# Performance work log

Hardware: AMD Instinct MI355X
Metric: run time of the kernel (lower is better)

## Reference

```python
import jax, jax.numpy as jnp
import numpy as np

N_ATOMS = 200000
N_BONDS = 400000
MAX_NB = 6
HID = 128
ATOM_FDIM = 151
BOND_FDIM = 165
N_HEADS = 2


def _layer_norm(x, g, b, eps=1e-5):
    mu = jnp.mean(x, axis=-1, keepdims=True)
    var = jnp.var(x, axis=-1, keepdims=True)
    return g * (x - mu) * jax.lax.rsqrt(var + eps) + b


def setup_inputs() -> dict:
    key = jax.random.key(0)
    ks = jax.random.split(key, 12)
    s = 0.05  # weight init scale
    return {
        'f_atoms': jax.random.normal(ks[0], (N_ATOMS, ATOM_FDIM), jnp.float32),
        'f_bonds': jax.random.normal(ks[1], (N_BONDS, BOND_FDIM), jnp.float32),
        'a2a': jax.random.randint(ks[2], (N_ATOMS, MAX_NB), 0, N_ATOMS, jnp.int32),
        'a2b': jax.random.randint(ks[3], (N_ATOMS, MAX_NB), 0, N_BONDS, jnp.int32),
        'W_i': jax.random.normal(ks[4], (ATOM_FDIM, HID), jnp.float32) * s,
        'b_i': jnp.zeros((HID,), jnp.float32),
        'ln1_g': jnp.ones((HID,), jnp.float32),
        'ln1_b': jnp.zeros((HID,), jnp.float32),
        'Wh_q': jax.random.normal(ks[5], (N_HEADS, HID + BOND_FDIM, HID), jnp.float32) * s,
        'bh_q': jnp.zeros((N_HEADS, HID), jnp.float32),
        'Wh_k': jax.random.normal(ks[6], (N_HEADS, HID + BOND_FDIM, HID), jnp.float32) * s,
        'bh_k': jnp.zeros((N_HEADS, HID), jnp.float32),
        'Wh_v': jax.random.normal(ks[7], (N_HEADS, HID + BOND_FDIM, HID), jnp.float32) * s,
        'bh_v': jnp.zeros((N_HEADS, HID), jnp.float32),
        'W_o': jax.random.normal(ks[8], (N_HEADS * HID, HID), jnp.float32) * s,
        'b_o': jnp.zeros((HID,), jnp.float32),
        'ln2_g': jnp.ones((HID,), jnp.float32),
        'ln2_b': jnp.zeros((HID,), jnp.float32),
    }


def reference(f_atoms, f_bonds, a2a, a2b, W_i, b_i, ln1_g, ln1_b,
              Wh_q, bh_q, Wh_k, bh_k, Wh_v, bh_v, W_o, b_o, ln2_g, ln2_b):
    # Input projection of raw atom features: dropout(layernorm(act(W_i x)))
    # (dropout = identity in eval).
    h0 = _layer_norm(jax.nn.relu(f_atoms @ W_i + b_i), ln1_g, ln1_b)  # [N, H]

    # Graph gather: neighbor atom hidden states + incident bond raw features.
    nei_a = h0[a2a]       # [N, nb, H]   irregular gather
    nei_b = f_bonds[a2b]  # [N, nb, Fb]  irregular gather
    # Aggregate messages once; shared across Q/K/V branches and heads.
    msg = jnp.concatenate([nei_a, nei_b], axis=-1).sum(axis=1)  # [N, H+Fb]

    def branch(Wh, bh):  # Wh: [heads, H+Fb, H] -> [N, heads, H]
        return jax.nn.relu(h0[:, None, :] + jnp.einsum('nf,efh->neh', msg, Wh) + bh)

    Q = branch(Wh_q, bh_q)  # [N, heads, H]
    K = branch(Wh_k, bh_k)
    V = branch(Wh_v, bh_v)

    # Attention across the heads axis (per atom).
    scores = jnp.einsum('nqh,nkh->nqk', Q, K) / jnp.sqrt(jnp.float32(HID))
    attn = jax.nn.softmax(scores, axis=-1)
    x = jnp.einsum('nqk,nkh->nqh', attn, V).reshape(Q.shape[0], -1)  # [N, heads*H]

    x_out = x @ W_o + b_o  # [N, H]
    # Residual sublayer connection.
    f_atoms_out = h0 + _layer_norm(x_out, ln2_g, ln2_b)
    return f_atoms_out
```

## Files before the change

kernel.cpp:

```cpp
#include <hip/hip_runtime.h>

typedef unsigned short u16;
typedef unsigned int u32;
typedef __attribute__((ext_vector_type(8))) short s8v;
typedef __attribute__((ext_vector_type(4))) float f4v;
typedef __attribute__((ext_vector_type(2))) float f2v;

#define NATOMS 200000
#define NBONDS 400000

__device__ __forceinline__ float b2f(u32 u) {
    union { u32 i; float f; } v; v.i = u << 16; return v.f;
}
__device__ __forceinline__ u16 f2b(float f) {
    union { float f; u32 i; } v; v.f = f;
    u32 r = v.i + 0x7fffu + ((v.i >> 16) & 1u);
    return (u16)(r >> 16);
}
__device__ __forceinline__ uint4 pack8(const float* f) {
    uint4 o;
    o.x = (u32)f2b(f[0]) | ((u32)f2b(f[1]) << 16);
    o.y = (u32)f2b(f[2]) | ((u32)f2b(f[3]) << 16);
    o.z = (u32)f2b(f[4]) | ((u32)f2b(f[5]) << 16);
    o.w = (u32)f2b(f[6]) | ((u32)f2b(f[7]) << 16);
    return o;
}
__device__ __forceinline__ void acc8(uint4 u, float* a) {
    a[0] += b2f(u.x & 0xffffu); a[1] += b2f(u.x >> 16);
    a[2] += b2f(u.y & 0xffffu); a[3] += b2f(u.y >> 16);
    a[4] += b2f(u.z & 0xffffu); a[5] += b2f(u.z >> 16);
    a[6] += b2f(u.w & 0xffffu); a[7] += b2f(u.w >> 16);
}

template<int C>
__device__ __forceinline__ float dpp_mov_f(float x) {
    return __int_as_float(__builtin_amdgcn_update_dpp(
        0, __float_as_int(x), C, 0xF, 0xF, true));
}
__device__ __forceinline__ float red8(float x) {
    x += dpp_mov_f<0xB1>(x);
    x += dpp_mov_f<0x4E>(x);
    x += dpp_mov_f<0x141>(x);
    return x;
}
__device__ __forceinline__ float red16(float x) {
    x += dpp_mov_f<0xB1>(x);
    x += dpp_mov_f<0x4E>(x);
    x += dpp_mov_f<0x141>(x);
    x += dpp_mov_f<0x128>(x);
    return x;
}

__global__ void k_wprep(const float* __restrict__ Whq, const float* __restrict__ Whk,
                        const float* __restrict__ Whv, const float* __restrict__ Wo,
                        const float* __restrict__ Wi,
                        u16* __restrict__ wallw, u16* __restrict__ wow, u16* __restrict__ wiw) {
    int t = blockIdx.x * 256 + threadIdx.x;
    if (t < 245760) {
        int ks = t / 24576, rem = t % 24576;
        int n = rem >> 5, kk = rem & 31;
        int k = ks * 32 + kk;
        int hg = n / 48, r48 = n % 48;
        int branch = r48 >> 4, r16i = r48 & 15;
        int head = r16i >> 3, h = hg * 8 + (r16i & 7);
        const float* Wp = (branch == 0) ? Whq : ((branch == 1) ? Whk : Whv);
        float val = (k < 293) ? Wp[(head * 293 + k) * 128 + h] : 0.f;
        wallw[t] = f2b(val);
    } else if (t < 278528) {
        int u = t - 245760;
        int ks = u >> 12, n = (u >> 5) & 127, kk = u & 31;
        int k = ks * 32 + kk;
        wow[u] = f2b(Wo[k * 128 + n]);
    } else if (t < 299008) {
        int u = t - 278528;
        int ks = u >> 12, n = (u >> 5) & 127, kk = u & 31;
        int k = ks * 32 + kk;
        wiw[u] = (k < 151) ? f2b(Wi[k * 128 + n]) : (u16)0;
    }
}

__global__ void k_bond16(const float* __restrict__ fb, u16* __restrict__ fbw) {
    int t = blockIdx.x * 256 + threadIdx.x;
    if (t >= NBONDS * 21) return;
    u32 b = (u32)t / 21u, c = (u32)t % 21u;
    const float* src = fb + (size_t)b * 165 + c * 8;
    float a[8];
    #pragma unroll
    for (int q = 0; q < 8; q++) a[q] = ((int)(c * 8 + q) < 165) ? src[q] : 0.f;
    *(uint4*)&fbw[(size_t)b * 168 + c * 8] = pack8(a);
}

__global__ void k_msgab(const u16* __restrict__ h0w, const int* __restrict__ a2a,
                        u16* __restrict__ msga,
                        const u16* __restrict__ fbw, const int* __restrict__ a2b,
                        u16* __restrict__ msgb) {
    if (blockIdx.x < 12500) {
        int t = blockIdx.x * 256 + threadIdx.x;
        if (t >= NATOMS * 16) return;
        u32 atom = (u32)t >> 4, c = (u32)t & 15u;
        const int* na = a2a + (size_t)atom * 6;
        float a[8] = {0, 0, 0, 0, 0, 0, 0, 0};
        #pragma unroll
        for (int j = 0; j < 6; j++)
            acc8(*(const uint4*)&h0w[(size_t)(u32)na[j] * 128 + c * 8], a);
        *(uint4*)&msga[(size_t)atom * 128 + c * 8] = pack8(a);
    } else {
        int t = (blockIdx.x - 12500) * 256 + threadIdx.x;
        if (t >= NATOMS * 21) return;
        u32 atom = (u32)t / 21u, c = (u32)t % 21u;
        const int* nb = a2b + (size_t)atom * 6;
        float a[8] = {0, 0, 0, 0, 0, 0, 0, 0};
        #pragma unroll
        for (int j = 0; j < 6; j++)
            acc8(*(const uint4*)&fbw[(size_t)(u32)nb[j] * 168 + c * 8], a);
        *(uint4*)&msgb[(size_t)atom * 168 + c * 8] = pack8(a);
    }
}

#define H0_SMEM (64 * 168 * 2 + 64 * 132 * 4)
__global__ __launch_bounds__(256) void k_h0(
    const float* __restrict__ fa, const u16* __restrict__ wiw,
    const float* __restrict__ bi, const float* __restrict__ g1, const float* __restrict__ b1,
    u16* __restrict__ h0w) {
    extern __shared__ char smem[];
    u16* la = (u16*)smem;
    float* lo = (float*)(smem + 21504);
    const int tid = threadIdx.x;
    const size_t abase = (size_t)blockIdx.x * 64;

    for (int i = tid; i < 64 * 151; i += 256) {
        int r = i / 151, c = i - r * 151;
        la[r * 168 + c] = f2b(fa[(abase + r) * 151 + c]);
    }
    for (int i = tid; i < 64 * 17; i += 256) {
        int r = i / 17, c = i - r * 17;
        la[r * 168 + 151 + c] = 0;
    }
    __syncthreads();

    const int w = tid >> 6, l = tid & 63;
    const int r16 = l & 15, kq = l >> 4;
    f4v acc[4][2];
    #pragma unroll
    for (int m = 0; m < 4; m++)
        #pragma unroll
        for (int c = 0; c < 2; c++)
            #pragma unroll
            for (int v = 0; v < 4; v++) acc[m][c][v] = 0.f;

    #pragma unroll
    for (int ks = 0; ks < 5; ++ks) {
        s8v af[4];
        #pragma unroll
        for (int m = 0; m < 4; m++)
            af[m] = *(const s8v*)&la[(m * 16 + r16) * 168 + ks * 32 + kq * 8];
        #pragma unroll
        for (int c = 0; c < 2; c++) {
            int n = w * 32 + c * 16 + r16;
            s8v bf = *(const s8v*)&wiw[ks * 4096 + n * 32 + kq * 8];
            #pragma unroll
            for (int m = 0; m < 4; m++)
                acc[m][c] = __builtin_amdgcn_mfma_f32_16x16x32_bf16(af[m], bf, acc[m][c], 0, 0, 0);
        }
    }
    #pragma unroll
    for (int c = 0; c < 2; c++) {
        int col = w * 32 + c * 16 + r16;
        float bias = bi[col];
        #pragma unroll
        for (int m = 0; m < 4; m++) {
            #pragma unroll
            for (int v = 0; v < 4; v++) {
                int row = m * 16 + kq * 4 + v;
                lo[row * 132 + col] = fmaxf(acc[m][c][v] + bias, 0.f);
            }
        }
    }
    __syncthreads();

    const int ga = tid >> 2, sb = tid & 3;
    float vals[32], s = 0.f, s2 = 0.f;
    #pragma unroll
    for (int j = 0; j < 32; j++) {
        float v = lo[ga * 132 + sb + 4 * j];
        vals[j] = v; s += v; s2 += v * v;
    }
    s += dpp_mov_f<0xB1>(s); s += dpp_mov_f<0x4E>(s);
    s2 += dpp_mov_f<0xB1>(s2); s2 += dpp_mov_f<0x4E>(s2);
    float mu = s * (1.f / 128.f), var = s2 * (1.f / 128.f) - mu * mu;
    float rs = rsqrtf(var + 1e-5f);
    u16* orow = h0w + (abase + ga) * 128;
    #pragma unroll
    for (int j = 0; j < 32; j++) {
        int col = sb + 4 * j;
        orow[col] = f2b(g1[col] * (vals[j] - mu) * rs + b1[col]);
    }
}

#define SMEM_FUSED 39936
__global__ __launch_bounds__(1024, 8) void k_fused(
    const u16* __restrict__ h0w, const u16* __restrict__ msga, const u16* __restrict__ msgb,
    const u16* __restrict__ wallw, const u16* __restrict__ wow,
    const float* __restrict__ bhq, const float* __restrict__ bhk, const float* __restrict__ bhv,
    const float* __restrict__ bo, const float* __restrict__ g2, const float* __restrict__ b2,
    float* __restrict__ out) {
    extern __shared__ char smem[];
    u16* lx = (u16*)smem;
    float* sco2 = (float*)(smem + 20480);
    u16* lh0 = (u16*)(smem + 28672);
    float* attn = (float*)(smem + 37376);
    float* pp = (float*)(smem + 37888);

    const int tid = threadIdx.x;
    const size_t abase = (size_t)blockIdx.x * 32;
    const int w = tid >> 6, l = tid & 63;
    const int r16 = l & 15, kq = l >> 4;
    const u32 xmask = (u32)((r16 & 7) << 4);

    const u16* bp = wallw + (size_t)(w * 48 + r16) * 32 + kq * 8;
    s8v bfA0 = *(const s8v*)&bp[0];
    s8v bfA1 = *(const s8v*)&bp[512];
    s8v bfA2 = *(const s8v*)&bp[1024];

    if (tid < 512) {
        int r = tid >> 4, c8 = tid & 15;
        *(uint4*)&lh0[r * 136 + c8 * 8] = *(const uint4*)&h0w[(abase + r) * 128 + c8 * 8];
    }

    #pragma unroll
    for (int ii = 0; ii < 2; ++ii) {
        int i = tid + ii * 1024;
        if (i < 1280) {
            int r = i / 40, c = i - r * 40;
            uint4 val;
            if (c < 16) {
                val = *(const uint4*)&msga[(abase + r) * 128 + c * 8];
            } else if (c < 37) {
                val = *(const uint4*)&msgb[(abase + r) * 168 + (c - 16) * 8];
            } else {
                val = (uint4){0, 0, 0, 0};
            }
            *(uint4*)(smem + (((u32)(r * 640 + c * 16)) ^ ((u32)((r & 7) << 4)))) = val;
        }
    }
    __syncthreads();

    f4v acc[2][3];
    #pragma unroll
    for (int m = 0; m < 2; m++)
        #pragma unroll
        for (int c = 0; c < 3; c++)
            #pragma unroll
            for (int v = 0; v < 4; v++) acc[m][c][v] = 0.f;

    s8v bfB0, bfB1, bfB2;
    #pragma unroll
    for (int kp = 0; kp < 5; ++kp) {
        {
            const int ks = 2 * kp;
            const u16* nb = bp + (size_t)(ks + 1) * 24576;
            bfB0 = *(const s8v*)&nb[0];
            bfB1 = *(const s8v*)&nb[512];
            bfB2 = *(const s8v*)&nb[1024];
            #pragma unroll
            for (int m = 0; m < 2; m++) {
                s8v af = *(const s8v*)(smem +
                    (((u32)((m * 16 + r16) * 640 + ks * 64 + kq * 16)) ^ xmask));
                acc[m][0] = __builtin_amdgcn_mfma_f32_16x16x32_bf16(af, bfA0, acc[m][0], 0, 0, 0);
                acc[m][1] = __builtin_amdgcn_mfma_f32_16x16x32_bf16(af, bfA1, acc[m][1], 0, 0, 0);
                acc[m][2] = __builtin_amdgcn_mfma_f32_16x16x32_bf16(af, bfA2, acc[m][2], 0, 0, 0);
            }
        }
        {
            const int ks = 2 * kp + 1;
            if (kp < 4) {
                const u16* nb = bp + (size_t)(ks + 1) * 24576;
                bfA0 = *(const s8v*)&nb[0];
                bfA1 = *(const s8v*)&nb[512];
                bfA2 = *(const s8v*)&nb[1024];
            }
            #pragma unroll
            for (int m = 0; m < 2; m++) {
                s8v af = *(const s8v*)(smem +
                    (((u32)((m * 16 + r16) * 640 + ks * 64 + kq * 16)) ^ xmask));
                acc[m][0] = __builtin_amdgcn_mfma_f32_16x16x32_bf16(af, bfB0, acc[m][0], 0, 0, 0);
                acc[m][1] = __builtin_amdgcn_mfma_f32_16x16x32_bf16(af, bfB1, acc[m][1], 0, 0, 0);
                acc[m][2] = __builtin_amdgcn_mfma_f32_16x16x32_bf16(af, bfB2, acc[m][2], 0, 0, 0);
            }
        }
    }

    const int head = r16 >> 3;
    const int h = w * 8 + (r16 & 7);
    const float bq = bhq[head * 128 + h];
    const float bk = bhk[head * 128 + h];
    const float bv = bhv[head * 128 + h];
    #pragma unroll
    for (int m = 0; m < 2; m++) {
        #pragma unroll
        for (int v = 0; v < 4; v++) {
            int row = m * 16 + kq * 4 + v;
            float h0v = b2f(lh0[row * 136 + h]);
            float q  = fmaxf(acc[m][0][v] + h0v + bq, 0.f);
            float kk = fmaxf(acc[m][1][v] + h0v + bk, 0.f);
            float vv = fmaxf(acc[m][2][v] + h0v + bv, 0.f);
            acc[m][2][v] = vv;
            float kx = dpp_mov_f<0x128>(kk);
            float pA = red8(q * kk);
            float pB = red8(q * kx);
            if ((r16 & 7) == (m * 4 + v)) {
                f2v pr; pr[0] = pA; pr[1] = pB;
                *(f2v*)&sco2[(w * 32 + row) * 4 + head * 2] = pr;
            }
        }
    }
    __syncthreads();

    if (tid < 64) {
        int atom = tid >> 1, qh = tid & 1;
        float ss = 0.f, sx = 0.f;
        #pragma unroll
        for (int ww = 0; ww < 16; ww++) {
            f2v p = *(const f2v*)&sco2[(ww * 32 + atom) * 4 + qh * 2];
            ss += p[0]; sx += p[1];
        }
        const float sc = 0.08838834764831845f;
        ss *= sc; sx *= sc;
        float mm = fmaxf(ss, sx);
        float e0 = __expf(ss - mm), e1 = __expf(sx - mm);
        float inv = 1.f / (e0 + e1);
        attn[atom * 4 + qh * 2] = e0 * inv;
        attn[atom * 4 + qh * 2 + 1] = e1 * inv;
    }
    __syncthreads();

    #pragma unroll
    for (int m = 0; m < 2; m++) {
        #pragma unroll
        for (int v = 0; v < 4; v++) {
            int row = m * 16 + kq * 4 + v;
            f2v a = *(const f2v*)&attn[row * 4 + head * 2];
            float vv = acc[m][2][v];
            float vx = dpp_mov_f<0x128>(vv);
            lx[row * 264 + head * 128 + h] = f2b(a[0] * vv + a[1] * vx);
        }
    }
    __syncthreads();

    const int mb = w >> 3, ch = w & 7;
    f4v oa;
    #pragma unroll
    for (int v = 0; v < 4; v++) oa[v] = 0.f;
    const u16* xp = lx + (mb * 16 + r16) * 264 + kq * 8;
    const u16* wp2 = wow + (ch * 16 + r16) * 32 + kq * 8;
    #pragma unroll
    for (int ks = 0; ks < 8; ks++) {
        s8v a = *(const s8v*)&xp[ks * 32];
        s8v b = *(const s8v*)&wp2[ks * 4096];
        oa = __builtin_amdgcn_mfma_f32_16x16x32_bf16(a, b, oa, 0, 0, 0);
    }

    const int col = ch * 16 + r16;
    const float boc = bo[col];
    float xo[4];
    #pragma unroll
    for (int v = 0; v < 4; v++) {
        xo[v] = oa[v] + boc;
        float s = red16(xo[v]);
        float s2 = red16(xo[v] * xo[v]);
        if (r16 == 0) {
            int row = mb * 16 + kq * 4 + v;
            f2v pr; pr[0] = s; pr[1] = s2;
            *(f2v*)&pp[(row * 8 + ch) * 2] = pr;
        }
    }
    __syncthreads();

    const float gac = g2[col], bbc = b2[col];
    #pragma unroll
    for (int v = 0; v < 4; v++) {
        int row = mb * 16 + kq * 4 + v;
        f4v p0 = *(f4v*)&pp[row * 16];
        f4v p1 = *(f4v*)&pp[row * 16 + 4];
        f4v p2 = *(f4v*)&pp[row * 16 + 8];
        f4v p3 = *(f4v*)&pp[row * 16 + 12];
        float ssum = p0[0] + p0[2] + p1[0] + p1[2] + p2[0] + p2[2] + p3[0] + p3[2];
        float s2sum = p0[1] + p0[3] + p1[1] + p1[3] + p2[1] + p2[3] + p3[1] + p3[3];
        float mu = ssum * (1.f / 128.f);
        float var = s2sum * (1.f / 128.f) - mu * mu;
        float rs = rsqrtf(var + 1e-5f);
        out[(abase + row) * 128 + col] =
            gac * (xo[v] - mu) * rs + bbc + b2f(lh0[row * 136 + col]);
    }
}

extern "C" void kernel_launch(void* const* d_in, const int* in_sizes, int n_in,
                              void* d_out, int out_size, void* d_ws, size_t ws_size,
                              hipStream_t stream) {
    const float* f_atoms = (const float*)d_in[0];
    const float* f_bonds = (const float*)d_in[1];
    const int* a2a = (const int*)d_in[2];
    const int* a2b = (const int*)d_in[3];
    const float* W_i = (const float*)d_in[4];
    const float* b_i = (const float*)d_in[5];
    const float* ln1g = (const float*)d_in[6];
    const float* ln1b = (const float*)d_in[7];
    const float* Whq = (const float*)d_in[8];
    const float* bhq = (const float*)d_in[9];
    const float* Whk = (const float*)d_in[10];
    const float* bhk = (const float*)d_in[11];
    const float* Whv = (const float*)d_in[12];
    const float* bhv = (const float*)d_in[13];
    const float* Wo = (const float*)d_in[14];
    const float* bo = (const float*)d_in[15];
    const float* ln2g = (const float*)d_in[16];
    const float* ln2b = (const float*)d_in[17];
    float* out = (float*)d_out;

    char* ws = (char*)d_ws;
    u16* h0w = (u16*)(ws + 0);
    u16* fbw = (u16*)(ws + 51200000);
    u16* msga = (u16*)(ws + 185600000);
    u16* msgb = (u16*)(ws + 236800000);
    u16* wallw = (u16*)(ws + 304000000);
    u16* wow = (u16*)(ws + 304491520);
    u16* wiw = (u16*)(ws + 304557056);

    hipFuncSetAttribute(reinterpret_cast<const void*>(k_fused),
                        hipFuncAttributeMaxDynamicSharedMemorySize, SMEM_FUSED);

    k_wprep<<<1168, 256, 0, stream>>>(Whq, Whk, Whv, Wo, W_i, wallw, wow, wiw);
    k_bond16<<<32813, 256, 0, stream>>>(f_bonds, fbw);
    k_h0<<<3125, 256, H0_SMEM, stream>>>(f_atoms, wiw, b_i, ln1g, ln1b, h0w);
    k_msgab<<<28907, 256, 0, stream>>>(h0w, a2a, msga, fbw, a2b, msgb);
    k_fused<<<6250, 1024, SMEM_FUSED, stream>>>(h0w, msga, msgb, wallw, wow,
                                                bhq, bhk, bhv, bo, ln2g, ln2b, out);
}
```

Baseline: 572.3 us.

## Process 48 atoms per block in fused kernel to amortize weight loads

```diff
diff --git a/kernel.cpp b/kernel.cpp
--- a/kernel.cpp
+++ b/kernel.cpp
@@ -37,16 +37,19 @@
     return __int_as_float(__builtin_amdgcn_update_dpp(
         0, __float_as_int(x), C, 0xF, 0xF, true));
 }
+__device__ __forceinline__ float swz_xor4(float x) {
+    return __int_as_float(__builtin_amdgcn_ds_swizzle(__float_as_int(x), 0x101F));
+}
 __device__ __forceinline__ float red8(float x) {
     x += dpp_mov_f<0xB1>(x);
     x += dpp_mov_f<0x4E>(x);
-    x += dpp_mov_f<0x141>(x);
+    x += swz_xor4(x);
     return x;
 }
 __device__ __forceinline__ float red16(float x) {
     x += dpp_mov_f<0xB1>(x);
     x += dpp_mov_f<0x4E>(x);
-    x += dpp_mov_f<0x141>(x);
+    x += swz_xor4(x);
     x += dpp_mov_f<0x128>(x);
     return x;
 }
@@ -197,7 +200,7 @@
     }
 }
 
-#define SMEM_FUSED 39936
+#define SMEM_FUSED 34560
 __global__ __launch_bounds__(1024, 8) void k_fused(
     const u16* __restrict__ h0w, const u16* __restrict__ msga, const u16* __restrict__ msgb,
     const u16* __restrict__ wallw, const u16* __restrict__ wow,
@@ -205,38 +208,28 @@
     const float* __restrict__ bo, const float* __restrict__ g2, const float* __restrict__ b2,
     float* __restrict__ out) {
     extern __shared__ char smem[];
+    float* sco2 = (float*)smem;
     u16* lx = (u16*)smem;
-    float* sco2 = (float*)(smem + 20480);
-    u16* lh0 = (u16*)(smem + 28672);
-    float* attn = (float*)(smem + 37376);
-    float* pp = (float*)(smem + 37888);
+    float* attn = (float*)(smem + 30720);
+    float* pp = (float*)(smem + 31488);
 
     const int tid = threadIdx.x;
-    const size_t abase = (size_t)blockIdx.x * 32;
+    const int abase = blockIdx.x * 48;
     const int w = tid >> 6, l = tid & 63;
     const int r16 = l & 15, kq = l >> 4;
     const u32 xmask = (u32)((r16 & 7) << 4);
 
-    const u16* bp = wallw + (size_t)(w * 48 + r16) * 32 + kq * 8;
-    s8v bfA0 = *(const s8v*)&bp[0];
-    s8v bfA1 = *(const s8v*)&bp[512];
-    s8v bfA2 = *(const s8v*)&bp[1024];
-
-    if (tid < 512) {
-        int r = tid >> 4, c8 = tid & 15;
-        *(uint4*)&lh0[r * 136 + c8 * 8] = *(const uint4*)&h0w[(abase + r) * 128 + c8 * 8];
-    }
-
     #pragma unroll
     for (int ii = 0; ii < 2; ++ii) {
         int i = tid + ii * 1024;
-        if (i < 1280) {
+        if (i < 1920) {
             int r = i / 40, c = i - r * 40;
+            int rr = abase + r; if (rr >= NATOMS) rr = NATOMS - 1;
             uint4 val;
             if (c < 16) {
-                val = *(const uint4*)&msga[(abase + r) * 128 + c * 8];
+                val = *(const uint4*)&msga[(size_t)rr * 128 + c * 8];
             } else if (c < 37) {
-                val = *(const uint4*)&msgb[(abase + r) * 168 + (c - 16) * 8];
+                val = *(const uint4*)&msgb[(size_t)rr * 168 + (c - 16) * 8];
             } else {
                 val = (uint4){0, 0, 0, 0};
             }
@@ -245,50 +238,31 @@
     }
     __syncthreads();
 
-    f4v acc[2][3];
-    #pragma unroll
-    for (int m = 0; m < 2; m++)
+    f4v acc[3][3];
+    #pragma unroll
+    for (int m = 0; m < 3; m++)
         #pragma unroll
         for (int c = 0; c < 3; c++)
             #pragma unroll
             for (int v = 0; v < 4; v++) acc[m][c][v] = 0.f;
 
-    s8v bfB0, bfB1, bfB2;
-    #pragma unroll
-    for (int kp = 0; kp < 5; ++kp) {
-        {
-            const int ks = 2 * kp;
-            const u16* nb = bp + (size_t)(ks + 1) * 24576;
-            bfB0 = *(const s8v*)&nb[0];
-            bfB1 = *(const s8v*)&nb[512];
-            bfB2 = *(const s8v*)&nb[1024];
-            #pragma unroll
-            for (int m = 0; m < 2; m++) {
-                s8v af = *(const s8v*)(smem +
-                    (((u32)((m * 16 + r16) * 640 + ks * 64 + kq * 16)) ^ xmask));
-                acc[m][0] = __builtin_amdgcn_mfma_f32_16x16x32_bf16(af, bfA0, acc[m][0], 0, 0, 0);
-                acc[m][1] = __builtin_amdgcn_mfma_f32_16x16x32_bf16(af, bfA1, acc[m][1], 0, 0, 0);
-                acc[m][2] = __builtin_amdgcn_mfma_f32_16x16x32_bf16(af, bfA2, acc[m][2], 0, 0, 0);
-            }
-        }
-        {
-            const int ks = 2 * kp + 1;
-            if (kp < 4) {
-                const u16* nb = bp + (size_t)(ks + 1) * 24576;
-                bfA0 = *(const s8v*)&nb[0];
-                bfA1 = *(const s8v*)&nb[512];
-                bfA2 = *(const s8v*)&nb[1024];
-            }
-            #pragma unroll
-            for (int m = 0; m < 2; m++) {
-                s8v af = *(const s8v*)(smem +
-                    (((u32)((m * 16 + r16) * 640 + ks * 64 + kq * 16)) ^ xmask));
-                acc[m][0] = __builtin_amdgcn_mfma_f32_16x16x32_bf16(af, bfB0, acc[m][0], 0, 0, 0);
-                acc[m][1] = __builtin_amdgcn_mfma_f32_16x16x32_bf16(af, bfB1, acc[m][1], 0, 0, 0);
-                acc[m][2] = __builtin_amdgcn_mfma_f32_16x16x32_bf16(af, bfB2, acc[m][2], 0, 0, 0);
-            }
-        }
-    }
+    const u16* bp = wallw + (size_t)(w * 48 + r16) * 32 + kq * 8;
+    #pragma unroll
+    for (int ks = 0; ks < 10; ++ks) {
+        const u16* nb = bp + (size_t)ks * 24576;
+        s8v b0 = *(const s8v*)&nb[0];
+        s8v b1 = *(const s8v*)&nb[512];
+        s8v b2_ = *(const s8v*)&nb[1024];
+        #pragma unroll
+        for (int m = 0; m < 3; m++) {
+            s8v af = *(const s8v*)(smem +
+                (((u32)((m * 16 + r16) * 640 + ks * 64 + kq * 16)) ^ xmask));
+            acc[m][0] = __builtin_amdgcn_mfma_f32_16x16x32_bf16(af, b0, acc[m][0], 0, 0, 0);
+            acc[m][1] = __builtin_amdgcn_mfma_f32_16x16x32_bf16(af, b1, acc[m][1], 0, 0, 0);
+            acc[m][2] = __builtin_amdgcn_mfma_f32_16x16x32_bf16(af, b2_, acc[m][2], 0, 0, 0);
+        }
+    }
+    __syncthreads();
 
     const int head = r16 >> 3;
     const int h = w * 8 + (r16 & 7);
@@ -296,11 +270,12 @@
     const float bk = bhk[head * 128 + h];
     const float bv = bhv[head * 128 + h];
     #pragma unroll
-    for (int m = 0; m < 2; m++) {
+    for (int m = 0; m < 3; m++) {
         #pragma unroll
         for (int v = 0; v < 4; v++) {
             int row = m * 16 + kq * 4 + v;
-            float h0v = b2f(lh0[row * 136 + h]);
+            int gr = abase + row; if (gr >= NATOMS) gr = NATOMS - 1;
+            float h0v = b2f(h0w[(size_t)gr * 128 + h]);
             float q  = fmaxf(acc[m][0][v] + h0v + bq, 0.f);
             float kk = fmaxf(acc[m][1][v] + h0v + bk, 0.f);
             float vv = fmaxf(acc[m][2][v] + h0v + bv, 0.f);
@@ -308,20 +283,20 @@
             float kx = dpp_mov_f<0x128>(kk);
             float pA = red8(q * kk);
             float pB = red8(q * kx);
-            if ((r16 & 7) == (m * 4 + v)) {
+            if ((r16 & 7) == ((m * 4 + v) & 7)) {
                 f2v pr; pr[0] = pA; pr[1] = pB;
-                *(f2v*)&sco2[(w * 32 + row) * 4 + head * 2] = pr;
-            }
-        }
-    }
-    __syncthreads();
-
-    if (tid < 64) {
+                *(f2v*)&sco2[(w * 48 + row) * 4 + head * 2] = pr;
+            }
+        }
+    }
+    __syncthreads();
+
+    if (tid < 96) {
         int atom = tid >> 1, qh = tid & 1;
         float ss = 0.f, sx = 0.f;
         #pragma unroll
         for (int ww = 0; ww < 16; ww++) {
-            f2v p = *(const f2v*)&sco2[(ww * 32 + atom) * 4 + qh * 2];
+            f2v p = *(const f2v*)&sco2[(ww * 48 + atom) * 4 + qh * 2];
             ss += p[0]; sx += p[1];
         }
         const float sc = 0.08838834764831845f;
@@ -335,7 +310,7 @@
     __syncthreads();
 
     #pragma unroll
-    for (int m = 0; m < 2; m++) {
+    for (int m = 0; m < 3; m++) {
         #pragma unroll
         for (int v = 0; v < 4; v++) {
             int row = m * 16 + kq * 4 + v;
@@ -347,50 +322,69 @@
     }
     __syncthreads();
 
-    const int mb = w >> 3, ch = w & 7;
-    f4v oa;
-    #pragma unroll
-    for (int v = 0; v < 4; v++) oa[v] = 0.f;
-    const u16* xp = lx + (mb * 16 + r16) * 264 + kq * 8;
+    const int ch = w & 7;
+    const int nmb = (w < 8) ? 2 : 1;
+    const int mb0 = (w < 8) ? 0 : 2;
+    f4v oa[2];
+    #pragma unroll
+    for (int v = 0; v < 4; v++) { oa[0][v] = 0.f; oa[1][v] = 0.f; }
     const u16* wp2 = wow + (ch * 16 + r16) * 32 + kq * 8;
     #pragma unroll
     for (int ks = 0; ks < 8; ks++) {
-        s8v a = *(const s8v*)&xp[ks * 32];
         s8v b = *(const s8v*)&wp2[ks * 4096];
-        oa = __builtin_amdgcn_mfma_f32_16x16x32_bf16(a, b, oa, 0, 0, 0);
+        #pragma unroll
+        for (int i = 0; i < 2; i++) {
+            if (i < nmb) {
+                s8v a = *(const s8v*)&lx[((mb0 + i) * 16 + r16) * 264 + ks * 32 + kq * 8];
+                oa[i] = __builtin_amdgcn_mfma_f32_16x16x32_bf16(a, b, oa[i], 0, 0, 0);
+            }
+        }
     }
 
     const int col = ch * 16 + r16;
     const float boc = bo[col];
-    float xo[4];
-    #pragma unroll
-    for (int v = 0; v < 4; v++) {
-        xo[v] = oa[v] + boc;
-        float s = red16(xo[v]);
-        float s2 = red16(xo[v] * xo[v]);
-        if (r16 == 0) {
-            int row = mb * 16 + kq * 4 + v;
-            f2v pr; pr[0] = s; pr[1] = s2;
-            *(f2v*)&pp[(row * 8 + ch) * 2] = pr;
+    float xo[2][4];
+    #pragma unroll
+    for (int i = 0; i < 2; i++) {
+        if (i < nmb) {
+            #pragma unroll
+            for (int v = 0; v < 4; v++) {
+                xo[i][v] = oa[i][v] + boc;
+                float s = red16(xo[i][v]);
+                float s2 = red16(xo[i][v] * xo[i][v]);
+                if (r16 == 0) {
+                    int row = (mb0 + i) * 16 + kq * 4 + v;
+                    f2v pr; pr[0] = s; pr[1] = s2;
+                    *(f2v*)&pp[(row * 8 + ch) * 2] = pr;
+                }
+            }
         }
     }
     __syncthreads();
 
     const float gac = g2[col], bbc = b2[col];
     #pragma unroll
-    for (int v = 0; v < 4; v++) {
-        int row = mb * 16 + kq * 4 + v;
-        f4v p0 = *(f4v*)&pp[row * 16];
-        f4v p1 = *(f4v*)&pp[row * 16 + 4];
-        f4v p2 = *(f4v*)&pp[row * 16 + 8];
-        f4v p3 = *(f4v*)&pp[row * 16 + 12];
-        float ssum = p0[0] + p0[2] + p1[0] + p1[2] + p2[0] + p2[2] + p3[0] + p3[2];
-        float s2sum = p0[1] + p0[3] + p1[1] + p1[3] + p2[1] + p2[3] + p3[1] + p3[3];
-        float mu = ssum * (1.f / 128.f);
-        float var = s2sum * (1.f / 128.f) - mu * mu;
-        float rs = rsqrtf(var + 1e-5f);
-        out[(abase + row) * 128 + col] =
-            gac * (xo[v] - mu) * rs + bbc + b2f(lh0[row * 136 + col]);
+    for (int i = 0; i < 2; i++) {
+        if (i < nmb) {
+            #pragma unroll
+            for (int v = 0; v < 4; v++) {
+                int row = (mb0 + i) * 16 + kq * 4 + v;
+                f4v p0 = *(f4v*)&pp[row * 16];
+                f4v p1 = *(f4v*)&pp[row * 16 + 4];
+                f4v p2 = *(f4v*)&pp[row * 16 + 8];
+                f4v p3 = *(f4v*)&pp[row * 16 + 12];
+                float ssum = p0[0] + p0[2] + p1[0] + p1[2] + p2[0] + p2[2] + p3[0] + p3[2];
+                float s2sum = p0[1] + p0[3] + p1[1] + p1[3] + p2[1] + p2[3] + p3[1] + p3[3];
+                float mu = ssum * (1.f / 128.f);
+                float var = s2sum * (1.f / 128.f) - mu * mu;
+                float rs = rsqrtf(var + 1e-5f);
+                int gr = abase + row;
+                if (gr < NATOMS) {
+                    out[(size_t)gr * 128 + col] =
+                        gac * (xo[i][v] - mu) * rs + bbc + b2f(h0w[(size_t)gr * 128 + col]);
+                }
+            }
+        }
     }
 }
 
@@ -433,6 +427,6 @@
     k_bond16<<<32813, 256, 0, stream>>>(f_bonds, fbw);
     k_h0<<<3125, 256, H0_SMEM, stream>>>(f_atoms, wiw, b_i, ln1g, ln1b, h0w);
     k_msgab<<<28907, 256, 0, stream>>>(h0w, a2a, msga, fbw, a2b, msgb);
-    k_fused<<<6250, 1024, SMEM_FUSED, stream>>>(h0w, msga, msgb, wallw, wow,
+    k_fused<<<4167, 1024, SMEM_FUSED, stream>>>(h0w, msga, msgb, wallw, wow,
                                                 bhq, bhk, bhv, bo, ln2g, ln2b, out);
 }
```

Measured after the change: 722.4 us. 26.2% more time.

## Merge prep kernels, do h0 layernorm in registers, shrink fused LDS footprint

Applied to the files above, without the earlier changes.

```diff
diff --git a/kernel.cpp b/kernel.cpp
--- a/kernel.cpp
+++ b/kernel.cpp
@@ -37,57 +37,61 @@
     return __int_as_float(__builtin_amdgcn_update_dpp(
         0, __float_as_int(x), C, 0xF, 0xF, true));
 }
+__device__ __forceinline__ float swz_xor4(float x) {
+    return __int_as_float(__builtin_amdgcn_ds_swizzle(__float_as_int(x), 0x101F));
+}
 __device__ __forceinline__ float red8(float x) {
     x += dpp_mov_f<0xB1>(x);
     x += dpp_mov_f<0x4E>(x);
-    x += dpp_mov_f<0x141>(x);
+    x += swz_xor4(x);
     return x;
 }
 __device__ __forceinline__ float red16(float x) {
     x += dpp_mov_f<0xB1>(x);
     x += dpp_mov_f<0x4E>(x);
-    x += dpp_mov_f<0x141>(x);
+    x += swz_xor4(x);
     x += dpp_mov_f<0x128>(x);
     return x;
 }
 
-__global__ void k_wprep(const float* __restrict__ Whq, const float* __restrict__ Whk,
-                        const float* __restrict__ Whv, const float* __restrict__ Wo,
-                        const float* __restrict__ Wi,
-                        u16* __restrict__ wallw, u16* __restrict__ wow, u16* __restrict__ wiw) {
-    int t = blockIdx.x * 256 + threadIdx.x;
-    if (t < 245760) {
-        int ks = t / 24576, rem = t % 24576;
-        int n = rem >> 5, kk = rem & 31;
-        int k = ks * 32 + kk;
-        int hg = n / 48, r48 = n % 48;
-        int branch = r48 >> 4, r16i = r48 & 15;
-        int head = r16i >> 3, h = hg * 8 + (r16i & 7);
-        const float* Wp = (branch == 0) ? Whq : ((branch == 1) ? Whk : Whv);
-        float val = (k < 293) ? Wp[(head * 293 + k) * 128 + h] : 0.f;
-        wallw[t] = f2b(val);
-    } else if (t < 278528) {
-        int u = t - 245760;
-        int ks = u >> 12, n = (u >> 5) & 127, kk = u & 31;
-        int k = ks * 32 + kk;
-        wow[u] = f2b(Wo[k * 128 + n]);
-    } else if (t < 299008) {
-        int u = t - 278528;
-        int ks = u >> 12, n = (u >> 5) & 127, kk = u & 31;
-        int k = ks * 32 + kk;
-        wiw[u] = (k < 151) ? f2b(Wi[k * 128 + n]) : (u16)0;
-    }
-}
-
-__global__ void k_bond16(const float* __restrict__ fb, u16* __restrict__ fbw) {
-    int t = blockIdx.x * 256 + threadIdx.x;
-    if (t >= NBONDS * 21) return;
-    u32 b = (u32)t / 21u, c = (u32)t % 21u;
-    const float* src = fb + (size_t)b * 165 + c * 8;
-    float a[8];
-    #pragma unroll
-    for (int q = 0; q < 8; q++) a[q] = ((int)(c * 8 + q) < 165) ? src[q] : 0.f;
-    *(uint4*)&fbw[(size_t)b * 168 + c * 8] = pack8(a);
+__global__ void k_prep(const float* __restrict__ Whq, const float* __restrict__ Whk,
+                       const float* __restrict__ Whv, const float* __restrict__ Wo,
+                       const float* __restrict__ Wi,
+                       u16* __restrict__ wallw, u16* __restrict__ wow, u16* __restrict__ wiw,
+                       const float* __restrict__ fb, u16* __restrict__ fbw) {
+    if (blockIdx.x < 1168) {
+        int t = blockIdx.x * 256 + threadIdx.x;
+        if (t < 245760) {
+            int ks = t / 24576, rem = t % 24576;
+            int n = rem >> 5, kk = rem & 31;
+            int k = ks * 32 + kk;
+            int hg = n / 48, r48 = n % 48;
+            int branch = r48 >> 4, r16i = r48 & 15;
+            int head = r16i >> 3, h = hg * 8 + (r16i & 7);
+            const float* Wp = (branch == 0) ? Whq : ((branch == 1) ? Whk : Whv);
+            float val = (k < 293) ? Wp[(head * 293 + k) * 128 + h] : 0.f;
+            wallw[t] = f2b(val);
+        } else if (t < 278528) {
+            int u = t - 245760;
+            int ks = u >> 12, n = (u >> 5) & 127, kk = u & 31;
+            int k = ks * 32 + kk;
+            wow[u] = f2b(Wo[k * 128 + n]);
+        } else if (t < 299008) {
+            int u = t - 278528;
+            int ks = u >> 12, n = (u >> 5) & 127, kk = u & 31;
+            int k = ks * 32 + kk;
+            wiw[u] = (k < 151) ? f2b(Wi[k * 128 + n]) : (u16)0;
+        }
+    } else {
+        int t = (blockIdx.x - 1168) * 256 + threadIdx.x;
+        if (t >= NBONDS * 21) return;
+        u32 b = (u32)t / 21u, c = (u32)t % 21u;
+        const float* src = fb + (size_t)b * 165 + c * 8;
+        float a[8];
+        #pragma unroll
+        for (int q = 0; q < 8; q++) a[q] = ((int)(c * 8 + q) < 165) ? src[q] : 0.f;
+        *(uint4*)&fbw[(size_t)b * 168 + c * 8] = pack8(a);
+    }
 }
 
 __global__ void k_msgab(const u16* __restrict__ h0w, const int* __restrict__ a2a,
@@ -117,14 +121,14 @@
     }
 }
 
-#define H0_SMEM (64 * 168 * 2 + 64 * 132 * 4)
+#define H0_SMEM 23552
 __global__ __launch_bounds__(256) void k_h0(
     const float* __restrict__ fa, const u16* __restrict__ wiw,
-    const float* __restrict__ bi, const float* __restrict__ g1, const float* __restrict__ b1,
+    const float* __restrict__ bi, const float* __restrict__ g1p, const float* __restrict__ b1p,
     u16* __restrict__ h0w) {
     extern __shared__ char smem[];
     u16* la = (u16*)smem;
-    float* lo = (float*)(smem + 21504);
+    float* pp = (float*)(smem + 21504);
     const int tid = threadIdx.x;
     const size_t abase = (size_t)blockIdx.x * 64;
 
@@ -163,41 +167,48 @@
                 acc[m][c] = __builtin_amdgcn_mfma_f32_16x16x32_bf16(af[m], bf, acc[m][c], 0, 0, 0);
         }
     }
-    #pragma unroll
-    for (int c = 0; c < 2; c++) {
-        int col = w * 32 + c * 16 + r16;
-        float bias = bi[col];
-        #pragma unroll
-        for (int m = 0; m < 4; m++) {
-            #pragma unroll
-            for (int v = 0; v < 4; v++) {
+
+    const int col0 = w * 32 + r16, col1 = col0 + 16;
+    const float bi0 = bi[col0], bi1 = bi[col1];
+    #pragma unroll
+    for (int m = 0; m < 4; m++) {
+        #pragma unroll
+        for (int v = 0; v < 4; v++) {
+            acc[m][0][v] = fmaxf(acc[m][0][v] + bi0, 0.f);
+            acc[m][1][v] = fmaxf(acc[m][1][v] + bi1, 0.f);
+            float s = red16(acc[m][0][v] + acc[m][1][v]);
+            float s2 = red16(acc[m][0][v] * acc[m][0][v] + acc[m][1][v] * acc[m][1][v]);
+            if (r16 == 0) {
                 int row = m * 16 + kq * 4 + v;
-                lo[row * 132 + col] = fmaxf(acc[m][c][v] + bias, 0.f);
-            }
-        }
-    }
-    __syncthreads();
-
-    const int ga = tid >> 2, sb = tid & 3;
-    float vals[32], s = 0.f, s2 = 0.f;
-    #pragma unroll
-    for (int j = 0; j < 32; j++) {
-        float v = lo[ga * 132 + sb + 4 * j];
-        vals[j] = v; s += v; s2 += v * v;
-    }
-    s += dpp_mov_f<0xB1>(s); s += dpp_mov_f<0x4E>(s);
-    s2 += dpp_mov_f<0xB1>(s2); s2 += dpp_mov_f<0x4E>(s2);
-    float mu = s * (1.f / 128.f), var = s2 * (1.f / 128.f) - mu * mu;
-    float rs = rsqrtf(var + 1e-5f);
-    u16* orow = h0w + (abase + ga) * 128;
-    #pragma unroll
-    for (int j = 0; j < 32; j++) {
-        int col = sb + 4 * j;
-        orow[col] = f2b(g1[col] * (vals[j] - mu) * rs + b1[col]);
-    }
-}
-
-#define SMEM_FUSED 39936
+                f2v pr; pr[0] = s; pr[1] = s2;
+                *(f2v*)&pp[(row * 4 + w) * 2] = pr;
+            }
+        }
+    }
+    __syncthreads();
+
+    const float g0 = g1p[col0], g1v = g1p[col1];
+    const float e0 = b1p[col0], e1 = b1p[col1];
+    #pragma unroll
+    for (int m = 0; m < 4; m++) {
+        #pragma unroll
+        for (int v = 0; v < 4; v++) {
+            int row = m * 16 + kq * 4 + v;
+            f4v p0 = *(f4v*)&pp[row * 8];
+            f4v p1 = *(f4v*)&pp[row * 8 + 4];
+            float ssum = p0[0] + p0[2] + p1[0] + p1[2];
+            float s2sum = p0[1] + p0[3] + p1[1] + p1[3];
+            float mu = ssum * (1.f / 128.f);
+            float var = s2sum * (1.f / 128.f) - mu * mu;
+            float rs = rsqrtf(var + 1e-5f);
+            u16* orow = h0w + (abase + row) * 128;
+            orow[col0] = f2b(g0 * (acc[m][0][v] - mu) * rs + e0);
+            orow[col1] = f2b(g1v * (acc[m][1][v] - mu) * rs + e1);
+        }
+    }
+}
+
+#define SMEM_FUSED 29184
 __global__ __launch_bounds__(1024, 8) void k_fused(
     const u16* __restrict__ h0w, const u16* __restrict__ msga, const u16* __restrict__ msgb,
     const u16* __restrict__ wallw, const u16* __restrict__ wow,
@@ -205,11 +216,11 @@
     const float* __restrict__ bo, const float* __restrict__ g2, const float* __restrict__ b2,
     float* __restrict__ out) {
     extern __shared__ char smem[];
+    float* sco2 = (float*)smem;
     u16* lx = (u16*)smem;
-    float* sco2 = (float*)(smem + 20480);
-    u16* lh0 = (u16*)(smem + 28672);
-    float* attn = (float*)(smem + 37376);
-    float* pp = (float*)(smem + 37888);
+    float* attn = (float*)(smem + 16896);
+    float* pp = (float*)(smem + 17408);
+    u16* lh0 = (u16*)(smem + 20480);
 
     const int tid = threadIdx.x;
     const size_t abase = (size_t)blockIdx.x * 32;
@@ -289,6 +300,7 @@
             }
         }
     }
+    __syncthreads();
 
     const int head = r16 >> 3;
     const int h = w * 8 + (r16 & 7);
@@ -429,8 +441,8 @@
     hipFuncSetAttribute(reinterpret_cast<const void*>(k_fused),
                         hipFuncAttributeMaxDynamicSharedMemorySize, SMEM_FUSED);
 
-    k_wprep<<<1168, 256, 0, stream>>>(Whq, Whk, Whv, Wo, W_i, wallw, wow, wiw);
-    k_bond16<<<32813, 256, 0, stream>>>(f_bonds, fbw);
+    k_prep<<<33981, 256, 0, stream>>>(Whq, Whk, Whv, Wo, W_i, wallw, wow, wiw,
+                                      f_bonds, fbw);
     k_h0<<<3125, 256, H0_SMEM, stream>>>(f_atoms, wiw, b_i, ln1g, ln1b, h0w);
     k_msgab<<<28907, 256, 0, stream>>>(h0w, a2a, msga, fbw, a2b, msgb);
     k_fused<<<6250, 1024, SMEM_FUSED, stream>>>(h0w, msga, msgb, wallw, wow,
```

Result: faster. 536.3 us (-6.3%).
